# Kernel optimization log

Hardware: AMD Instinct MI355X
Metric: run time of the kernel (lower is better)

Reference implementation:

```python
import jax, jax.numpy as jnp
import numpy as np

B, N, F = 4, 1024, 256
AVG_DEG = 16.0


def setup_inputs() -> dict:
    key = jax.random.key(0)
    k1, k2, k3, k4 = jax.random.split(key, 4)
    u = jax.random.uniform(k1, (B, N, N))
    A = (u < AVG_DEG / N).astype(jnp.float32)
    A = jnp.maximum(A, jnp.swapaxes(A, 1, 2))            # symmetric
    A = A * (1.0 - jnp.eye(N, dtype=jnp.float32))        # no self loops (added in forward)
    x = jax.random.normal(k2, (B, N, F), dtype=jnp.float32)
    pos = jax.random.normal(k3, (B, N, 3), dtype=jnp.float32)
    order = jax.random.uniform(k4, (B, N), dtype=jnp.float32)  # 'random' ordering priorities
    node_mask = jnp.ones((B, N), dtype=bool)
    return {"x": x, "adj": A, "pos": pos, "order": order, "node_mask": node_mask}


def _select(order, excluded, included, node_mask):
    # Greedy frontier-based node selection (K-MIS with stride=2).
    Bn, Nn = order.shape
    ar = jnp.arange(Nn)
    idx0 = jnp.argmin(order, axis=-1).astype(jnp.int32)           # [B]
    available = node_mask
    frontier = ar[None, :] == idx0[:, None]                        # scatter idx0 -> True
    selected = jnp.zeros_like(available)

    def cond(st):
        av, fr, sel, idx = st
        return av.any()

    def body(st):
        av, fr, sel, idx = st
        current = ar[None, :] == idx[:, None]                      # [B,N] one-hot
        sel = sel | current
        exc_row = jnp.take_along_axis(excluded, idx[:, None, None], axis=1)[:, 0]  # excluded[current]
        inc_row = jnp.take_along_axis(included, idx[:, None, None], axis=1)[:, 0]  # included[current]
        av = av & ~current & ~exc_row
        fr = (fr | inc_row | ~fr.any(-1, keepdims=True)) & av      # restart frontier if empty
        mo = jnp.where(fr, order, jnp.inf)
        midx = jnp.argmin(mo, axis=-1).astype(jnp.int32)
        has_fr = fr.any(-1)
        idx = jnp.where(has_fr, midx, idx)
        return (av, fr, sel, idx)

    _, _, selected, _ = jax.lax.while_loop(cond, body, (available, frontier, selected, idx0))
    return selected


def _forward(x, adj, pos, order, node_mask):
    Nn = adj.shape[1]
    eye = jnp.eye(Nn, dtype=adj.dtype)
    adj1 = jnp.where(node_mask[:, :, None], adj + eye, 0.0)        # adj_k[1] = A + I, masked rows
    adj2 = adj1 @ adj                                              # adj_k[2] = (A+I) @ A
    excluded = adj1 != 0                                           # adj_k[stride-1].bool()
    included = adj2 != 0                                           # adj_k[stride].bool()
    selected = _select(jax.lax.stop_gradient(order), excluded, included, node_mask)
    # pad K to N instead of data-dependent num_nodes; mask zeroes the padding
    mask_f, perm = jax.lax.top_k(selected.astype(jnp.float32), Nn)  # [B,K], [B,K]
    adj_kernel = jnp.take_along_axis(adj1, perm[:, None, :], axis=2)  # [B,N,K]
    # add_pool: adj^T @ x, then mask
    x_p = jnp.einsum('bnk,bnf->bkf', adj_kernel, x) * mask_f[..., None]
    # mean_pool for pos: add_pool / column degree
    deg = adj_kernel.sum(axis=1)[..., None]                        # [B,K,1]
    pos_p = jnp.einsum('bnk,bnc->bkc', adj_kernel, pos) / deg * mask_f[..., None]
    # coarsened adjacency: gather cols then rows of adj_k[stride], mask both sides
    a = jnp.take_along_axis(adj2, perm[:, None, :], axis=2)
    a = jnp.take_along_axis(a, perm[:, :, None], axis=1)
    a = a * mask_f[:, None, :] * mask_f[:, :, None]
    return x_p, pos_p, a, mask_f.astype(bool)


def reference(x, adj, pos, order, node_mask):
    return _forward(x, adj, pos, order, node_mask)
```

## Files before the change

### kernel.cpp

```cpp
#include <hip/hip_runtime.h>
#include <hip/hip_bf16.h>

#define BB 4
#define NN 1024
#define FF 256
#define NBLK 1024
#define NTHR 256
#define PBLK 512
#define QN   504
#define QPOOL 3584
#define SROWS 128

typedef __hip_bfloat16 bf16;
typedef unsigned long long u64;
typedef unsigned int u32;
typedef unsigned short u16;
typedef unsigned char u8;

__device__ __forceinline__ bf16 f2b(float v) { return __float2bfloat16(v); }
__device__ __forceinline__ u16 f2bbits(float v) {
    bf16 h = __float2bfloat16(v);
    u16 s; __builtin_memcpy(&s, &h, 2);
    return s;
}
template <typename OT> __device__ __forceinline__ OT fromf(float v);
template <> __device__ __forceinline__ float fromf<float>(float v) { return v; }
template <> __device__ __forceinline__ bf16 fromf<bf16>(float v) { return __float2bfloat16(v); }

__device__ __forceinline__ void st_wt(u32* p, u32 v)   { __hip_atomic_store(p, v, __ATOMIC_RELAXED, __HIP_MEMORY_SCOPE_SYSTEM); }
__device__ __forceinline__ void st_wt(u64* p, u64 v)   { __hip_atomic_store(p, v, __ATOMIC_RELAXED, __HIP_MEMORY_SCOPE_SYSTEM); }
__device__ __forceinline__ void st_wt(int* p, int v)   { __hip_atomic_store(p, v, __ATOMIC_RELAXED, __HIP_MEMORY_SCOPE_SYSTEM); }
__device__ __forceinline__ void st_wt(float* p, float v){ __hip_atomic_store(p, v, __ATOMIC_RELAXED, __HIP_MEMORY_SCOPE_SYSTEM); }

__device__ __forceinline__ void tree_sync(int* reg, int idx, int ngroups, int phase) {
    __syncthreads();
    if (threadIdx.x == 0) {
        asm volatile("s_waitcnt vmcnt(0)" ::: "memory");
        int* gc = reg + 32 * (9 + (idx >> 4));
        int v = __hip_atomic_fetch_add(gc, 1, __ATOMIC_RELAXED, __HIP_MEMORY_SCOPE_AGENT);
        if (v == phase * 16 - 1) {
            int r = __hip_atomic_fetch_add(reg, 1, __ATOMIC_RELAXED, __HIP_MEMORY_SCOPE_AGENT);
            if (r == phase * ngroups - 1)
                for (int xx = 0; xx < 8; xx++)
                    __hip_atomic_store(reg + 32 * (1 + xx), phase,
                                       __ATOMIC_RELAXED, __HIP_MEMORY_SCOPE_AGENT);
        }
        int* flag = reg + 32 * (1 + (idx & 7));
        int spins = 0;
        while (__hip_atomic_load(flag, __ATOMIC_RELAXED, __HIP_MEMORY_SCOPE_AGENT) < phase) {
            if (spins < 64) __builtin_amdgcn_s_sleep(2);
            else            __builtin_amdgcn_s_sleep(16);
            if (++spins > (1 << 20)) break;
        }
        asm volatile("" ::: "memory");
    }
    __syncthreads();
}

__device__ __forceinline__ int build_nbr(const u64* myrow, u16* nbr, int* cntp, int t) {
    __syncthreads();
    if (t < 16) {
        int myc = __popcll(myrow[t]);
        int ps = myc;
#pragma unroll
        for (int off = 1; off < 16; off <<= 1) {
            int v = __shfl_up(ps, off);
            if (t >= off) ps += v;
        }
        int idx = ps - myc;
        u64 m = myrow[t];
        while (m) {
            int i = __ffsll(m) - 1;
            if (idx < 192) nbr[idx] = (u16)(t * 64 + i);
            idx++;
            m &= m - 1;
        }
        if (t == 15) *cntp = ps;
    }
    __syncthreads();
    return min(*cntp, 192);
}

__device__ __forceinline__ void pool_task(int b, int n,
        const float* __restrict__ x, const float* __restrict__ pos,
        const u64* myrow, u16* nbr, int* cntp,
        float* __restrict__ xpool, float* __restrict__ pospool, int t) {
    const int c = build_nbr(myrow, nbr, cntp, t);
    const float* xr = x + (size_t)b * NN * FF;
    float acc = xr[(size_t)n * FF + t];
    int i = 0;
    for (; i + 4 <= c; i += 4) {
        float a0 = xr[(size_t)nbr[i + 0] * FF + t];
        float a1 = xr[(size_t)nbr[i + 1] * FF + t];
        float a2 = xr[(size_t)nbr[i + 2] * FF + t];
        float a3 = xr[(size_t)nbr[i + 3] * FF + t];
        acc += a0; acc += a1; acc += a2; acc += a3;
    }
    for (; i < c; i++) acc += xr[(size_t)nbr[i] * FF + t];
    st_wt(&xpool[((size_t)b * NN + n) * FF + t], acc);
    if (t < 3) {
        const size_t pb_ = (size_t)b * NN * 3;
        float pa = pos[pb_ + n * 3 + t];
        for (int j = 0; j < c; j++) pa += pos[pb_ + nbr[j] * 3 + t];
        st_wt(&pospool[((size_t)b * NN + n) * 4 + t], pa / (float)(c + 1));
    }
    __syncthreads();
}

template <typename OT>
__global__ __launch_bounds__(NTHR, 4) void mega_kernel(
        const float* __restrict__ x, const float* __restrict__ adj,
        const float* __restrict__ pos, const float* __restrict__ order,
        u64* __restrict__ bitsA, u32* __restrict__ packed,
        int* __restrict__ sp2node, int* __restrict__ node2sp,
        int* __restrict__ perm, int* __restrict__ kcnt,
        float* __restrict__ xpool, float* __restrict__ pospool,
        int* __restrict__ sink, int* __restrict__ bar,
        OT* __restrict__ out, size_t out_elems)
{
    const int B = blockIdx.x, t = threadIdx.x;
    __shared__ union ShU {
        u64 keys[NN];
        struct {
            u64 myrow[16], incw[16], part[256];
            int s2nT[16 * 65];
            u16 nbr[192];
            int cnt;
        } pb;
        struct {
            u64 myrow[16];
            u16 nbr[192];
            int cnt;
        } pl;
        struct {
            u32 stage[SROWS * 64];
            u8 selS[NN];
        } pc;
        struct {
            int p[NN];
            u64 myrow[16];
            u16 sta[NN];
        } pd;
    } sh;

    int* Greg = bar;
    int* Preg = bar + 32 * 73;
    int* srt  = bar + 32 * 114;

    if (B < PBLK) {
        const int b = B >> 7, rbase = (B * 8) & (NN - 1);
        for (int i = 0; i < 8; i++) {
            const int r = rbase + i;
            const size_t base = (size_t)b * NN * NN + (size_t)r * NN;
            for (int q = 0; q < 4; q++) {
                int j = q * 256 + t;
                u64 bal = __ballot(adj[base + j] != 0.0f);
                if ((t & 63) == 0) st_wt(&bitsA[((size_t)b * NN + r) * 16 + (j >> 6)], bal);
            }
        }
        tree_sync(Preg, B, 32, 1);
        if (t == 0) {
            int spins = 0;
            while (__hip_atomic_load(srt, __ATOMIC_RELAXED, __HIP_MEMORY_SCOPE_AGENT) < 8) {
                __builtin_amdgcn_s_sleep(2);
                if (++spins > (1 << 20)) break;
            }
            asm volatile("" ::: "memory");
        }
        __syncthreads();

        for (int q = 0; q < 4; q++) {
            int j = q * 256 + t;
            sh.pb.s2nT[(j & 15) * 65 + (j >> 4)] = sp2node[b * NN + j];
        }
        for (int rr = 0; rr < 8; rr++) {
            const int r = rbase + rr;
            if (t < 16) sh.pb.myrow[t] = bitsA[((size_t)b * NN + r) * 16 + t];
            const int c = build_nbr(sh.pb.myrow, sh.pb.nbr, &sh.pb.cnt, t);
            {
                const int w = t & 15, g = t >> 4;
                u64 v = 0;
                for (int n2 = g; n2 < c; n2 += 16)
                    v |= bitsA[((size_t)b * NN + sh.pb.nbr[n2]) * 16 + w];
                sh.pb.part[t] = v;
            }
            __syncthreads();
            if (t < 16) {
                u64 acc = sh.pb.myrow[t];
                for (int g = 0; g < 16; g++) acc |= sh.pb.part[g * 16 + t];
                sh.pb.incw[t] = acc;
            }
            __syncthreads();
            if (t < 64) {
                const int s = node2sp[b * NN + r];
                u32 e16 = 0, i16 = 0;
                for (int q = 0; q < 16; q++) {
                    int jn = sh.pb.s2nT[q * 65 + t];
                    u32 eb = (u32)((sh.pb.myrow[jn >> 6] >> (jn & 63)) & 1) | (u32)(jn == r);
                    u32 ib = (u32)((sh.pb.incw[jn >> 6] >> (jn & 63)) & 1);
                    e16 |= eb << q;
                    i16 |= ib << q;
                }
                st_wt(&packed[((size_t)b * NN + s) * 64 + t], e16 | (i16 << 16));
            }
            __syncthreads();
        }
        tree_sync(Preg, B, 32, 2);

        if (B < 4) {
            const int sb = B;
            const u32* pk = packed + (size_t)sb * NN * 64;
            u32 acc = 0;
            for (int i = t; i < NN * 16; i += NTHR) {
                uint4 v = ((const uint4*)pk)[i];
                if ((i >> 4) < SROWS) ((uint4*)sh.pc.stage)[i] = v;
                acc ^= v.x ^ v.y ^ v.z ^ v.w;
            }
            if (acc == 0xDEADBEEFu) atomicAdd(sink, 1);
            __syncthreads();

            if (t < 64) {
                const int l = t;
                u32 avail = 0xFFFFu, front = (l == 0) ? 1u : 0u, sel = 0u;
                int cur = 0;
                for (int iter = 0; iter < 2 * NN + 8; ++iter) {
                    if ((cur >> 4) == l) sel |= 1u << (cur & 15);
                    u32 p;
                    if (cur < SROWS) p = sh.pc.stage[cur * 64 + l];
                    else             p = pk[(size_t)cur * 64 + l];
                    avail &= ~(p & 0xFFFFu);
                    front = (front | (p >> 16)) & avail;
                    u64 fb = __ballot(front != 0u);
                    if (!fb) {
                        front = avail;
                        fb = __ballot(front != 0u);
                        if (!fb) break;
                    }
                    int lf = __ffsll(fb) - 1;
                    u32 f = (u32)__builtin_amdgcn_readlane((int)front, lf);
                    cur = lf * 16 + (__ffs(f) - 1);
                }
                for (int q = 0; q < 16; q++) sh.pc.selS[l * 16 + q] = (sel >> q) & 1u;
            }
            __syncthreads();
            if (t < 64) {
                const int l = t;
                u32 nodesel = 0;
                const int* n2s = node2sp + sb * NN;
                for (int q = 0; q < 16; q++)
                    nodesel |= ((u32)sh.pc.selS[n2s[l * 16 + q]]) << q;
                int cnt_sel = __popc(nodesel);
                int ps = cnt_sel;
                for (int off = 1; off < 64; off <<= 1) {
                    int v = __shfl_up(ps, off);
                    if (l >= off) ps += v;
                }
                const int K = __shfl(ps, 63);
                int pos_ = ps - cnt_sel;
                u32 m = nodesel;
                while (m) { int i = __ffs(m) - 1; st_wt(&perm[sb * NN + pos_], l * 16 + i); pos_++; m &= m - 1; }
                int posu = K + l * 16 - (ps - cnt_sel);
                m = (~nodesel) & 0xFFFFu;
                while (m) { int i = __ffs(m) - 1; st_wt(&perm[sb * NN + posu], l * 16 + i); posu++; m &= m - 1; }
                if (l == 0) st_wt(&kcnt[sb], K);
            }
        } else {
            for (int task = QPOOL + (B - 4); task < BB * NN; task += PBLK - 4) {
                const int tb = task & 3, n = task >> 2;
                if (t < 16) sh.pl.myrow[t] = bitsA[((size_t)tb * NN + n) * 16 + t];
                pool_task(tb, n, x, pos, sh.pl.myrow, sh.pl.nbr, &sh.pl.cnt,
                          xpool, pospool, t);
            }
        }
    } else if (B < PBLK + QN) {
        const int zi = B - PBLK;
        const size_t nb8 = (out_elems * sizeof(OT)) >> 3;
        u64* o8 = (u64*)out;
        for (size_t i = (size_t)zi * NTHR + t; i < nb8; i += (size_t)QN * NTHR)
            st_wt(o8 + i, (u64)0);
        for (int task = zi; task < QPOOL; task += QN) {
            const int tb = task & 3, n = task >> 2;
            const size_t abase = (size_t)tb * NN * NN + (size_t)n * NN;
            for (int q = 0; q < 4; q++) {
                int j = q * 256 + t;
                u64 bal = __ballot(adj[abase + j] != 0.0f);
                if ((t & 63) == 0) sh.pl.myrow[j >> 6] = bal;
            }
            pool_task(tb, n, x, pos, sh.pl.myrow, sh.pl.nbr, &sh.pl.cnt,
                      xpool, pospool, t);
        }
    } else {
        const int b = (B - (PBLK + QN)) >> 1, half = (B - (PBLK + QN)) & 1;
        for (int i = t; i < NN; i += NTHR) {
            float v = order[(size_t)b * NN + i];
            u32 ub = __float_as_uint(v);
            u32 sk = (ub & 0x80000000u) ? ~ub : (ub | 0x80000000u);
            sh.keys[i] = ((u64)sk << 32) | (u32)i;
        }
        __syncthreads();
        u64 mk0 = sh.keys[half * 512 + t], mk1 = sh.keys[half * 512 + 256 + t];
        int r0 = 0, r1 = 0;
        for (int m = 0; m < NN; m++) {
            u64 v = sh.keys[m];
            r0 += (v < mk0);
            r1 += (v < mk1);
        }
        int n0 = (int)(mk0 & 0xFFFFFFFFu), n1 = (int)(mk1 & 0xFFFFFFFFu);
        st_wt(&sp2node[b * NN + r0], n0); st_wt(&node2sp[b * NN + n0], r0);
        st_wt(&sp2node[b * NN + r1], n1); st_wt(&node2sp[b * NN + n1], r1);
        __syncthreads();
        if (t == 0)
            __hip_atomic_fetch_add(srt, 1, __ATOMIC_RELAXED, __HIP_MEMORY_SCOPE_AGENT);
    }

    tree_sync(Greg, B, 64, 1);

    OT* out_x = out;
    OT* out_pos = out_x + (size_t)BB * NN * FF;
    OT* out_a = out_pos + (size_t)BB * NN * 3;
    OT* out_mask = out_a + (size_t)BB * NN * NN;

    for (int task = B; task < BB * NN; task += NBLK) {
        const int b = task & 3, k = task >> 2;
        const int K = kcnt[b];
        if (k >= K) continue;
        const int r = perm[b * NN + k];
        OT* ox = out_x + ((size_t)b * NN + k) * FF;
        OT* op = out_pos + ((size_t)b * NN + k) * 3;
        OT* oa = out_a + ((size_t)b * NN + k) * NN;
        if (t == 0) out_mask[(size_t)b * NN + k] = fromf<OT>(1.0f);
        if (t < 16) sh.pd.myrow[t] = bitsA[((size_t)b * NN + r) * 16 + t];
        for (int q = 0; q < 4; q++) { int j = t + q * 256; sh.pd.p[j] = perm[b * NN + j]; }
        __syncthreads();

        if constexpr (sizeof(OT) == 2) {
            if (t < 32) {
                const float* xr = xpool + ((size_t)b * NN + r) * FF + t * 8;
                union { u16 w[8]; uint4 v; } u;
#pragma unroll
                for (int i = 0; i < 8; i++) u.w[i] = f2bbits(xr[i]);
                ((uint4*)ox)[t] = u.v;
            }
        } else {
            ox[t] = (OT)xpool[((size_t)b * NN + r) * FF + t];
        }
        if (t < 3) op[t] = fromf<OT>(pospool[((size_t)b * NN + r) * 4 + t]);

        if constexpr (sizeof(OT) == 2) {
            for (int q = 0; q < 4; q++) {
                int jj = t + q * 256;
                float v = 0.0f;
                if (jj < K) {
                    const int pj = sh.pd.p[jj];
                    const u64* rj = bitsA + ((size_t)b * NN + pj) * 16;
                    int a2 = (int)((sh.pd.myrow[pj >> 6] >> (pj & 63)) & 1);
#pragma unroll
                    for (int w = 0; w < 16; w++)
                        a2 += __popcll(sh.pd.myrow[w] & rj[w]);
                    v = (float)a2;
                }
                sh.pd.sta[jj] = f2bbits(v);
            }
            __syncthreads();
            const int nu = (K + 7) >> 3;
            if (t < nu) ((uint4*)oa)[t] = ((const uint4*)sh.pd.sta)[t];
            __syncthreads();
        } else {
            for (int q = 0; q < 4; q++) {
                int jj = t + q * 256;
                if (jj < K) {
                    const int pj = sh.pd.p[jj];
                    const u64* rj = bitsA + ((size_t)b * NN + pj) * 16;
                    int a2 = (int)((sh.pd.myrow[pj >> 6] >> (pj & 63)) & 1);
#pragma unroll
                    for (int w = 0; w < 16; w++)
                        a2 += __popcll(sh.pd.myrow[w] & rj[w]);
                    oa[jj] = (float)a2;
                }
            }
            __syncthreads();
        }
    }
}

extern "C" void kernel_launch(void* const* d_in, const int* in_sizes, int n_in,
                              void* d_out, int out_size, void* d_ws, size_t ws_size,
                              hipStream_t stream) {
    const float* x     = (const float*)d_in[0];
    const float* adj   = (const float*)d_in[1];
    const float* pos   = (const float*)d_in[2];
    const float* order = (const float*)d_in[3];

    char* ws = (char*)d_ws;
    size_t off = 0;
    u64* bitsA     = (u64*)(ws + off);  off += (size_t)BB * NN * 16 * 8;
    u32* packed    = (u32*)(ws + off);  off += (size_t)BB * NN * 64 * 4;
    int* sp2node   = (int*)(ws + off);  off += (size_t)BB * NN * 4;
    int* node2sp   = (int*)(ws + off);  off += (size_t)BB * NN * 4;
    int* perm      = (int*)(ws + off);  off += (size_t)BB * NN * 4;
    int* kcnt      = (int*)(ws + off);  off += 64;
    int* sink      = (int*)(ws + off);  off += 64;
    float* xpool   = (float*)(ws + off); off += (size_t)BB * NN * FF * 4;
    float* pospool = (float*)(ws + off); off += (size_t)BB * NN * 4 * 4;
    int* bar       = (int*)(ws + off);  off += 16384;

    hipMemsetAsync(bar, 0, 16384, stream);

    bool outf32 = false;
    size_t osz = 0;
    if (hipMemPtrGetInfo(d_out, &osz) == hipSuccess)
        outf32 = (osz >= 4ull * (size_t)out_size);

    if (outf32)
        mega_kernel<float><<<NBLK, NTHR, 0, stream>>>(x, adj, pos, order, bitsA, packed,
            sp2node, node2sp, perm, kcnt, xpool, pospool, sink, bar,
            (float*)d_out, (size_t)out_size);
    else
        mega_kernel<bf16><<<NBLK, NTHR, 0, stream>>>(x, adj, pos, order, bitsA, packed,
            sp2node, node2sp, perm, kcnt, xpool, pospool, sink, bar,
            (bf16*)d_out, (size_t)out_size);
}
```

Baseline: 158.3 us.

## Pool only selected nodes in output phase and spread bitmask build across all blocks

The separate pooling pass that computed x/pos aggregates for every node into workspace buffers is removed. Pooling is now done only for selected nodes, inside the final output loop, with a block-wide partial reduction for pos. The adjacency bitmask build and the incidence packing are spread over all 1024 blocks with a single grid barrier scheme, replacing the specialised block roles. Idle blocks prefetch x and bitsA slices to warm the cache while the four selection blocks run. The cost is that pooling now sits on the critical path after the serial selection, and the grid now passes through three barriers.

```diff
diff --git a/kernel.cpp b/kernel.cpp
--- a/kernel.cpp
+++ b/kernel.cpp
@@ -6,9 +6,6 @@
 #define FF 256
 #define NBLK 1024
 #define NTHR 256
-#define PBLK 512
-#define QN   504
-#define QPOOL 3584
 #define SROWS 128
 
 typedef __hip_bfloat16 bf16;
@@ -32,7 +29,7 @@
 __device__ __forceinline__ void st_wt(int* p, int v)   { __hip_atomic_store(p, v, __ATOMIC_RELAXED, __HIP_MEMORY_SCOPE_SYSTEM); }
 __device__ __forceinline__ void st_wt(float* p, float v){ __hip_atomic_store(p, v, __ATOMIC_RELAXED, __HIP_MEMORY_SCOPE_SYSTEM); }
 
-__device__ __forceinline__ void tree_sync(int* reg, int idx, int ngroups, int phase) {
+__device__ __forceinline__ void tree_sync(int* reg, int idx, int phase) {
     __syncthreads();
     if (threadIdx.x == 0) {
         asm volatile("s_waitcnt vmcnt(0)" ::: "memory");
@@ -40,7 +37,7 @@
         int v = __hip_atomic_fetch_add(gc, 1, __ATOMIC_RELAXED, __HIP_MEMORY_SCOPE_AGENT);
         if (v == phase * 16 - 1) {
             int r = __hip_atomic_fetch_add(reg, 1, __ATOMIC_RELAXED, __HIP_MEMORY_SCOPE_AGENT);
-            if (r == phase * ngroups - 1)
+            if (r == phase * 64 - 1)
                 for (int xx = 0; xx < 8; xx++)
                     __hip_atomic_store(reg + 32 * (1 + xx), phase,
                                        __ATOMIC_RELAXED, __HIP_MEMORY_SCOPE_AGENT);
@@ -50,7 +47,7 @@
         while (__hip_atomic_load(flag, __ATOMIC_RELAXED, __HIP_MEMORY_SCOPE_AGENT) < phase) {
             if (spins < 64) __builtin_amdgcn_s_sleep(2);
             else            __builtin_amdgcn_s_sleep(16);
-            if (++spins > (1 << 20)) break;
+            if (++spins > (1 << 19)) break;
         }
         asm volatile("" ::: "memory");
     }
@@ -81,32 +78,6 @@
     return min(*cntp, 192);
 }
 
-__device__ __forceinline__ void pool_task(int b, int n,
-        const float* __restrict__ x, const float* __restrict__ pos,
-        const u64* myrow, u16* nbr, int* cntp,
-        float* __restrict__ xpool, float* __restrict__ pospool, int t) {
-    const int c = build_nbr(myrow, nbr, cntp, t);
-    const float* xr = x + (size_t)b * NN * FF;
-    float acc = xr[(size_t)n * FF + t];
-    int i = 0;
-    for (; i + 4 <= c; i += 4) {
-        float a0 = xr[(size_t)nbr[i + 0] * FF + t];
-        float a1 = xr[(size_t)nbr[i + 1] * FF + t];
-        float a2 = xr[(size_t)nbr[i + 2] * FF + t];
-        float a3 = xr[(size_t)nbr[i + 3] * FF + t];
-        acc += a0; acc += a1; acc += a2; acc += a3;
-    }
-    for (; i < c; i++) acc += xr[(size_t)nbr[i] * FF + t];
-    st_wt(&xpool[((size_t)b * NN + n) * FF + t], acc);
-    if (t < 3) {
-        const size_t pb_ = (size_t)b * NN * 3;
-        float pa = pos[pb_ + n * 3 + t];
-        for (int j = 0; j < c; j++) pa += pos[pb_ + nbr[j] * 3 + t];
-        st_wt(&pospool[((size_t)b * NN + n) * 4 + t], pa / (float)(c + 1));
-    }
-    __syncthreads();
-}
-
 template <typename OT>
 __global__ __launch_bounds__(NTHR, 4) void mega_kernel(
         const float* __restrict__ x, const float* __restrict__ adj,
@@ -114,12 +85,11 @@
         u64* __restrict__ bitsA, u32* __restrict__ packed,
         int* __restrict__ sp2node, int* __restrict__ node2sp,
         int* __restrict__ perm, int* __restrict__ kcnt,
-        float* __restrict__ xpool, float* __restrict__ pospool,
         int* __restrict__ sink, int* __restrict__ bar,
         OT* __restrict__ out, size_t out_elems)
 {
     const int B = blockIdx.x, t = threadIdx.x;
-    __shared__ union ShU {
+    __shared__ alignas(16) union ShU {
         u64 keys[NN];
         struct {
             u64 myrow[16], incw[16], part[256];
@@ -128,171 +98,26 @@
             int cnt;
         } pb;
         struct {
-            u64 myrow[16];
-            u16 nbr[192];
-            int cnt;
-        } pl;
-        struct {
             u32 stage[SROWS * 64];
             u8 selS[NN];
         } pc;
         struct {
             int p[NN];
             u64 myrow[16];
+            u16 stx[FF];
             u16 sta[NN];
+            float posp[64][3];
+            u16 nbr[192];
+            int cnt;
         } pd;
     } sh;
 
-    int* Greg = bar;
-    int* Preg = bar + 32 * 73;
-    int* srt  = bar + 32 * 114;
-
-    if (B < PBLK) {
-        const int b = B >> 7, rbase = (B * 8) & (NN - 1);
-        for (int i = 0; i < 8; i++) {
-            const int r = rbase + i;
-            const size_t base = (size_t)b * NN * NN + (size_t)r * NN;
-            for (int q = 0; q < 4; q++) {
-                int j = q * 256 + t;
-                u64 bal = __ballot(adj[base + j] != 0.0f);
-                if ((t & 63) == 0) st_wt(&bitsA[((size_t)b * NN + r) * 16 + (j >> 6)], bal);
-            }
-        }
-        tree_sync(Preg, B, 32, 1);
-        if (t == 0) {
-            int spins = 0;
-            while (__hip_atomic_load(srt, __ATOMIC_RELAXED, __HIP_MEMORY_SCOPE_AGENT) < 8) {
-                __builtin_amdgcn_s_sleep(2);
-                if (++spins > (1 << 20)) break;
-            }
-            asm volatile("" ::: "memory");
-        }
-        __syncthreads();
-
-        for (int q = 0; q < 4; q++) {
-            int j = q * 256 + t;
-            sh.pb.s2nT[(j & 15) * 65 + (j >> 4)] = sp2node[b * NN + j];
-        }
-        for (int rr = 0; rr < 8; rr++) {
-            const int r = rbase + rr;
-            if (t < 16) sh.pb.myrow[t] = bitsA[((size_t)b * NN + r) * 16 + t];
-            const int c = build_nbr(sh.pb.myrow, sh.pb.nbr, &sh.pb.cnt, t);
-            {
-                const int w = t & 15, g = t >> 4;
-                u64 v = 0;
-                for (int n2 = g; n2 < c; n2 += 16)
-                    v |= bitsA[((size_t)b * NN + sh.pb.nbr[n2]) * 16 + w];
-                sh.pb.part[t] = v;
-            }
-            __syncthreads();
-            if (t < 16) {
-                u64 acc = sh.pb.myrow[t];
-                for (int g = 0; g < 16; g++) acc |= sh.pb.part[g * 16 + t];
-                sh.pb.incw[t] = acc;
-            }
-            __syncthreads();
-            if (t < 64) {
-                const int s = node2sp[b * NN + r];
-                u32 e16 = 0, i16 = 0;
-                for (int q = 0; q < 16; q++) {
-                    int jn = sh.pb.s2nT[q * 65 + t];
-                    u32 eb = (u32)((sh.pb.myrow[jn >> 6] >> (jn & 63)) & 1) | (u32)(jn == r);
-                    u32 ib = (u32)((sh.pb.incw[jn >> 6] >> (jn & 63)) & 1);
-                    e16 |= eb << q;
-                    i16 |= ib << q;
-                }
-                st_wt(&packed[((size_t)b * NN + s) * 64 + t], e16 | (i16 << 16));
-            }
-            __syncthreads();
-        }
-        tree_sync(Preg, B, 32, 2);
-
-        if (B < 4) {
-            const int sb = B;
-            const u32* pk = packed + (size_t)sb * NN * 64;
-            u32 acc = 0;
-            for (int i = t; i < NN * 16; i += NTHR) {
-                uint4 v = ((const uint4*)pk)[i];
-                if ((i >> 4) < SROWS) ((uint4*)sh.pc.stage)[i] = v;
-                acc ^= v.x ^ v.y ^ v.z ^ v.w;
-            }
-            if (acc == 0xDEADBEEFu) atomicAdd(sink, 1);
-            __syncthreads();
-
-            if (t < 64) {
-                const int l = t;
-                u32 avail = 0xFFFFu, front = (l == 0) ? 1u : 0u, sel = 0u;
-                int cur = 0;
-                for (int iter = 0; iter < 2 * NN + 8; ++iter) {
-                    if ((cur >> 4) == l) sel |= 1u << (cur & 15);
-                    u32 p;
-                    if (cur < SROWS) p = sh.pc.stage[cur * 64 + l];
-                    else             p = pk[(size_t)cur * 64 + l];
-                    avail &= ~(p & 0xFFFFu);
-                    front = (front | (p >> 16)) & avail;
-                    u64 fb = __ballot(front != 0u);
-                    if (!fb) {
-                        front = avail;
-                        fb = __ballot(front != 0u);
-                        if (!fb) break;
-                    }
-                    int lf = __ffsll(fb) - 1;
-                    u32 f = (u32)__builtin_amdgcn_readlane((int)front, lf);
-                    cur = lf * 16 + (__ffs(f) - 1);
-                }
-                for (int q = 0; q < 16; q++) sh.pc.selS[l * 16 + q] = (sel >> q) & 1u;
-            }
-            __syncthreads();
-            if (t < 64) {
-                const int l = t;
-                u32 nodesel = 0;
-                const int* n2s = node2sp + sb * NN;
-                for (int q = 0; q < 16; q++)
-                    nodesel |= ((u32)sh.pc.selS[n2s[l * 16 + q]]) << q;
-                int cnt_sel = __popc(nodesel);
-                int ps = cnt_sel;
-                for (int off = 1; off < 64; off <<= 1) {
-                    int v = __shfl_up(ps, off);
-                    if (l >= off) ps += v;
-                }
-                const int K = __shfl(ps, 63);
-                int pos_ = ps - cnt_sel;
-                u32 m = nodesel;
-                while (m) { int i = __ffs(m) - 1; st_wt(&perm[sb * NN + pos_], l * 16 + i); pos_++; m &= m - 1; }
-                int posu = K + l * 16 - (ps - cnt_sel);
-                m = (~nodesel) & 0xFFFFu;
-                while (m) { int i = __ffs(m) - 1; st_wt(&perm[sb * NN + posu], l * 16 + i); posu++; m &= m - 1; }
-                if (l == 0) st_wt(&kcnt[sb], K);
-            }
-        } else {
-            for (int task = QPOOL + (B - 4); task < BB * NN; task += PBLK - 4) {
-                const int tb = task & 3, n = task >> 2;
-                if (t < 16) sh.pl.myrow[t] = bitsA[((size_t)tb * NN + n) * 16 + t];
-                pool_task(tb, n, x, pos, sh.pl.myrow, sh.pl.nbr, &sh.pl.cnt,
-                          xpool, pospool, t);
-            }
-        }
-    } else if (B < PBLK + QN) {
-        const int zi = B - PBLK;
-        const size_t nb8 = (out_elems * sizeof(OT)) >> 3;
-        u64* o8 = (u64*)out;
-        for (size_t i = (size_t)zi * NTHR + t; i < nb8; i += (size_t)QN * NTHR)
-            st_wt(o8 + i, (u64)0);
-        for (int task = zi; task < QPOOL; task += QN) {
-            const int tb = task & 3, n = task >> 2;
-            const size_t abase = (size_t)tb * NN * NN + (size_t)n * NN;
-            for (int q = 0; q < 4; q++) {
-                int j = q * 256 + t;
-                u64 bal = __ballot(adj[abase + j] != 0.0f);
-                if ((t & 63) == 0) sh.pl.myrow[j >> 6] = bal;
-            }
-            pool_task(tb, n, x, pos, sh.pl.myrow, sh.pl.nbr, &sh.pl.cnt,
-                      xpool, pospool, t);
-        }
-    } else {
-        const int b = (B - (PBLK + QN)) >> 1, half = (B - (PBLK + QN)) & 1;
+    const int b = B >> 8, rbase = (B & 255) * 4;
+
+    if (B >= NBLK - 8) {
+        const int sb = (B - (NBLK - 8)) >> 1, half = (B - (NBLK - 8)) & 1;
         for (int i = t; i < NN; i += NTHR) {
-            float v = order[(size_t)b * NN + i];
+            float v = order[(size_t)sb * NN + i];
             u32 ub = __float_as_uint(v);
             u32 sk = (ub & 0x80000000u) ? ~ub : (ub | 0x80000000u);
             sh.keys[i] = ((u64)sk << 32) | (u32)i;
@@ -305,15 +130,136 @@
             r0 += (v < mk0);
             r1 += (v < mk1);
         }
-        int n0 = (int)(mk0 & 0xFFFFFFFFu), n1 = (int)(mk1 & 0xFFFFFFFFu);
-        st_wt(&sp2node[b * NN + r0], n0); st_wt(&node2sp[b * NN + n0], r0);
-        st_wt(&sp2node[b * NN + r1], n1); st_wt(&node2sp[b * NN + n1], r1);
-        __syncthreads();
-        if (t == 0)
-            __hip_atomic_fetch_add(srt, 1, __ATOMIC_RELAXED, __HIP_MEMORY_SCOPE_AGENT);
-    }
-
-    tree_sync(Greg, B, 64, 1);
+        int n0 = (int)(mk0 & 0xFFFFFFFFu) & (NN - 1), n1 = (int)(mk1 & 0xFFFFFFFFu) & (NN - 1);
+        r0 &= (NN - 1); r1 &= (NN - 1);
+        st_wt(&sp2node[sb * NN + r0], n0); st_wt(&node2sp[sb * NN + n0], r0);
+        st_wt(&sp2node[sb * NN + r1], n1); st_wt(&node2sp[sb * NN + n1], r1);
+        __syncthreads();
+    }
+
+    for (int rr = 0; rr < 4; rr++) {
+        const int r = rbase + rr;
+        const size_t base = (size_t)b * NN * NN + (size_t)r * NN;
+        for (int q = 0; q < 4; q++) {
+            int j = q * 256 + t;
+            u64 bal = __ballot(adj[base + j] != 0.0f);
+            if ((t & 63) == 0) st_wt(&bitsA[((size_t)b * NN + r) * 16 + (j >> 6)], bal);
+        }
+    }
+    tree_sync(bar, B, 1);
+
+    for (int q = 0; q < 4; q++) {
+        int j = q * 256 + t;
+        sh.pb.s2nT[(j & 15) * 65 + (j >> 4)] = sp2node[b * NN + j] & (NN - 1);
+    }
+    for (int rr = 0; rr < 4; rr++) {
+        const int r = rbase + rr;
+        if (t < 16) sh.pb.myrow[t] = bitsA[((size_t)b * NN + r) * 16 + t];
+        const int c = build_nbr(sh.pb.myrow, sh.pb.nbr, &sh.pb.cnt, t);
+        {
+            const int w = t & 15, g = t >> 4;
+            u64 v = 0;
+            for (int n2 = g; n2 < c; n2 += 16)
+                v |= bitsA[((size_t)b * NN + sh.pb.nbr[n2]) * 16 + w];
+            sh.pb.part[t] = v;
+        }
+        __syncthreads();
+        if (t < 16) {
+            u64 acc = sh.pb.myrow[t];
+            for (int g = 0; g < 16; g++) acc |= sh.pb.part[g * 16 + t];
+            sh.pb.incw[t] = acc;
+        }
+        __syncthreads();
+        if (t < 64) {
+            const int s = node2sp[b * NN + r] & (NN - 1);
+            u32 e16 = 0, i16 = 0;
+            for (int q = 0; q < 16; q++) {
+                int jn = sh.pb.s2nT[q * 65 + t];
+                u32 eb = (u32)((sh.pb.myrow[jn >> 6] >> (jn & 63)) & 1) | (u32)(jn == r);
+                u32 ib = (u32)((sh.pb.incw[jn >> 6] >> (jn & 63)) & 1);
+                e16 |= eb << q;
+                i16 |= ib << q;
+            }
+            st_wt(&packed[((size_t)b * NN + s) * 64 + t], e16 | (i16 << 16));
+        }
+        __syncthreads();
+    }
+    tree_sync(bar, B, 2);
+
+    if (B < 4) {
+        const int sb = B;
+        const u32* pk = packed + (size_t)sb * NN * 64;
+        u32 acc = 0;
+        for (int i = t; i < NN * 16; i += NTHR) {
+            uint4 v = ((const uint4*)pk)[i];
+            if ((i >> 4) < SROWS) ((uint4*)sh.pc.stage)[i] = v;
+            acc ^= v.x ^ v.y ^ v.z ^ v.w;
+        }
+        if (acc == 0xDEADBEEFu) atomicAdd(sink, 1);
+        __syncthreads();
+
+        if (t < 64) {
+            const int l = t;
+            u32 avail = 0xFFFFu, front = (l == 0) ? 1u : 0u, sel = 0u;
+            int cur = 0;
+            for (int iter = 0; iter < 2 * NN + 8; ++iter) {
+                if ((cur >> 4) == l) sel |= 1u << (cur & 15);
+                u32 p;
+                if (cur < SROWS) p = sh.pc.stage[cur * 64 + l];
+                else             p = pk[(size_t)cur * 64 + l];
+                avail &= ~(p & 0xFFFFu);
+                front = (front | (p >> 16)) & avail;
+                u64 fb = __ballot(front != 0u);
+                if (!fb) {
+                    front = avail;
+                    fb = __ballot(front != 0u);
+                    if (!fb) break;
+                }
+                int lf = __ffsll(fb) - 1;
+                u32 f = __shfl(front, lf);
+                cur = (lf * 16 + (__ffs(f) - 1)) & (NN - 1);
+            }
+            for (int q = 0; q < 16; q++) sh.pc.selS[l * 16 + q] = (sel >> q) & 1u;
+        }
+        __syncthreads();
+        if (t < 64) {
+            const int l = t;
+            u32 nodesel = 0;
+            const int* n2s = node2sp + sb * NN;
+            for (int q = 0; q < 16; q++)
+                nodesel |= ((u32)sh.pc.selS[n2s[l * 16 + q] & (NN - 1)]) << q;
+            int cnt_sel = __popc(nodesel);
+            int ps = cnt_sel;
+            for (int off = 1; off < 64; off <<= 1) {
+                int v = __shfl_up(ps, off);
+                if (l >= off) ps += v;
+            }
+            const int K = __shfl(ps, 63);
+            int pos_ = (ps - cnt_sel) & (NN - 1);
+            u32 m = nodesel;
+            while (m) { int i = __ffs(m) - 1; st_wt(&perm[sb * NN + pos_], l * 16 + i); pos_ = (pos_ + 1) & (NN - 1); m &= m - 1; }
+            int posu = (K + l * 16 - (ps - cnt_sel)) & (NN - 1);
+            m = (~nodesel) & 0xFFFFu;
+            while (m) { int i = __ffs(m) - 1; st_wt(&perm[sb * NN + posu], l * 16 + i); posu = (posu + 1) & (NN - 1); m &= m - 1; }
+            if (l == 0) st_wt(&kcnt[sb], K);
+        }
+    } else {
+        const size_t nb8 = (out_elems * sizeof(OT)) >> 3;
+        u64* o8 = (u64*)out;
+        for (size_t i = (size_t)(B - 4) * NTHR + t; i < nb8; i += (size_t)(NBLK - 4) * NTHR)
+            st_wt(o8 + i, (u64)0);
+        u32 acc = 0;
+        const int slot = B >> 3;
+        const uint4* xs = (const uint4*)x + (size_t)slot * 2048;
+        for (int i = t; i < 2048; i += NTHR) {
+            uint4 v = xs[i];
+            acc ^= v.x ^ v.y ^ v.z ^ v.w;
+        }
+        const u64* bs = bitsA + (size_t)slot * 512;
+        for (int i = t; i < 512; i += NTHR) acc ^= (u32)bs[i];
+        if (acc == 0xDEADBEEFu) atomicAdd(sink, 1);
+    }
+    tree_sync(bar, B, 3);
 
     OT* out_x = out;
     OT* out_pos = out_x + (size_t)BB * NN * FF;
@@ -321,38 +267,48 @@
     OT* out_mask = out_a + (size_t)BB * NN * NN;
 
     for (int task = B; task < BB * NN; task += NBLK) {
-        const int b = task & 3, k = task >> 2;
-        const int K = kcnt[b];
+        const int b2 = task & 3, k = task >> 2;
+        const int K = min(kcnt[b2], NN);
         if (k >= K) continue;
-        const int r = perm[b * NN + k];
-        OT* ox = out_x + ((size_t)b * NN + k) * FF;
-        OT* op = out_pos + ((size_t)b * NN + k) * 3;
-        OT* oa = out_a + ((size_t)b * NN + k) * NN;
-        if (t == 0) out_mask[(size_t)b * NN + k] = fromf<OT>(1.0f);
-        if (t < 16) sh.pd.myrow[t] = bitsA[((size_t)b * NN + r) * 16 + t];
-        for (int q = 0; q < 4; q++) { int j = t + q * 256; sh.pd.p[j] = perm[b * NN + j]; }
-        __syncthreads();
+        const int r = perm[b2 * NN + k] & (NN - 1);
+        OT* ox = out_x + ((size_t)b2 * NN + k) * FF;
+        OT* op = out_pos + ((size_t)b2 * NN + k) * 3;
+        OT* oa = out_a + ((size_t)b2 * NN + k) * NN;
+        if (t == 0) out_mask[(size_t)b2 * NN + k] = fromf<OT>(1.0f);
+        if (t < 16) sh.pd.myrow[t] = bitsA[((size_t)b2 * NN + r) * 16 + t];
+        for (int q = 0; q < 4; q++) { int j = t + q * 256; sh.pd.p[j] = perm[b2 * NN + j] & (NN - 1); }
+        const int c = build_nbr(sh.pd.myrow, sh.pd.nbr, &sh.pd.cnt, t);
+
+        const float* xr = x + (size_t)b2 * NN * FF;
+        float acc = xr[(size_t)r * FF + t];
+        int i = 0;
+        for (; i + 4 <= c; i += 4) {
+            float a0 = xr[(size_t)sh.pd.nbr[i + 0] * FF + t];
+            float a1 = xr[(size_t)sh.pd.nbr[i + 1] * FF + t];
+            float a2 = xr[(size_t)sh.pd.nbr[i + 2] * FF + t];
+            float a3 = xr[(size_t)sh.pd.nbr[i + 3] * FF + t];
+            acc += a0; acc += a1; acc += a2; acc += a3;
+        }
+        for (; i < c; i++) acc += xr[(size_t)sh.pd.nbr[i] * FF + t];
+
+        if (t < 64) {
+            float p0 = 0.0f, p1 = 0.0f, p2 = 0.0f;
+            const float* pr = pos + (size_t)b2 * NN * 3;
+            for (int n = t; n < c; n += 64) {
+                const float* pp = pr + (size_t)sh.pd.nbr[n] * 3;
+                p0 += pp[0]; p1 += pp[1]; p2 += pp[2];
+            }
+            sh.pd.posp[t][0] = p0; sh.pd.posp[t][1] = p1; sh.pd.posp[t][2] = p2;
+        }
 
         if constexpr (sizeof(OT) == 2) {
-            if (t < 32) {
-                const float* xr = xpool + ((size_t)b * NN + r) * FF + t * 8;
-                union { u16 w[8]; uint4 v; } u;
-#pragma unroll
-                for (int i = 0; i < 8; i++) u.w[i] = f2bbits(xr[i]);
-                ((uint4*)ox)[t] = u.v;
-            }
-        } else {
-            ox[t] = (OT)xpool[((size_t)b * NN + r) * FF + t];
-        }
-        if (t < 3) op[t] = fromf<OT>(pospool[((size_t)b * NN + r) * 4 + t]);
-
-        if constexpr (sizeof(OT) == 2) {
+            sh.pd.stx[t] = f2bbits(acc);
             for (int q = 0; q < 4; q++) {
                 int jj = t + q * 256;
                 float v = 0.0f;
                 if (jj < K) {
                     const int pj = sh.pd.p[jj];
-                    const u64* rj = bitsA + ((size_t)b * NN + pj) * 16;
+                    const u64* rj = bitsA + ((size_t)b2 * NN + pj) * 16;
                     int a2 = (int)((sh.pd.myrow[pj >> 6] >> (pj & 63)) & 1);
 #pragma unroll
                     for (int w = 0; w < 16; w++)
@@ -362,21 +318,36 @@
                 sh.pd.sta[jj] = f2bbits(v);
             }
             __syncthreads();
+            if (t < 3) {
+                const float* pr = pos + (size_t)b2 * NN * 3;
+                float pa = pr[(size_t)r * 3 + t];
+                for (int g = 0; g < 64; g++) pa += sh.pd.posp[g][t];
+                op[t] = fromf<OT>(pa / (float)(c + 1));
+            }
             const int nu = (K + 7) >> 3;
             if (t < nu) ((uint4*)oa)[t] = ((const uint4*)sh.pd.sta)[t];
+            if (t < 32) ((uint4*)ox)[t] = ((const uint4*)sh.pd.stx)[t];
             __syncthreads();
         } else {
+            ox[t] = acc;
             for (int q = 0; q < 4; q++) {
                 int jj = t + q * 256;
                 if (jj < K) {
                     const int pj = sh.pd.p[jj];
-                    const u64* rj = bitsA + ((size_t)b * NN + pj) * 16;
+                    const u64* rj = bitsA + ((size_t)b2 * NN + pj) * 16;
                     int a2 = (int)((sh.pd.myrow[pj >> 6] >> (pj & 63)) & 1);
 #pragma unroll
                     for (int w = 0; w < 16; w++)
                         a2 += __popcll(sh.pd.myrow[w] & rj[w]);
                     oa[jj] = (float)a2;
                 }
+            }
+            __syncthreads();
+            if (t < 3) {
+                const float* pr = pos + (size_t)b2 * NN * 3;
+                float pa = pr[(size_t)r * 3 + t];
+                for (int g = 0; g < 64; g++) pa += sh.pd.posp[g][t];
+                op[t] = fromf<OT>(pa / (float)(c + 1));
             }
             __syncthreads();
         }
@@ -400,8 +371,6 @@
     int* perm      = (int*)(ws + off);  off += (size_t)BB * NN * 4;
     int* kcnt      = (int*)(ws + off);  off += 64;
     int* sink      = (int*)(ws + off);  off += 64;
-    float* xpool   = (float*)(ws + off); off += (size_t)BB * NN * FF * 4;
-    float* pospool = (float*)(ws + off); off += (size_t)BB * NN * 4 * 4;
     int* bar       = (int*)(ws + off);  off += 16384;
 
     hipMemsetAsync(bar, 0, 16384, stream);
@@ -413,10 +382,8 @@
 
     if (outf32)
         mega_kernel<float><<<NBLK, NTHR, 0, stream>>>(x, adj, pos, order, bitsA, packed,
-            sp2node, node2sp, perm, kcnt, xpool, pospool, sink, bar,
-            (float*)d_out, (size_t)out_size);
+            sp2node, node2sp, perm, kcnt, sink, bar, (float*)d_out, (size_t)out_size);
     else
         mega_kernel<bf16><<<NBLK, NTHR, 0, stream>>>(x, adj, pos, order, bitsA, packed,
-            sp2node, node2sp, perm, kcnt, xpool, pospool, sink, bar,
-            (bf16*)d_out, (size_t)out_size);
-}
+            sp2node, node2sp, perm, kcnt, sink, bar, (bf16*)d_out, (size_t)out_size);
+}
```

New measurement: 166.1 us. +4.9%, slower.
